# Kernel tuning notes

Measured on AMD Instinct MI355X. Metric: run time of the kernel, lower is better.

Reference implementation:

```python
import jax, jax.numpy as jnp
import numpy as np

N_HEADS = 16
K_CH = 1024 // N_HEADS  # 64
SCALE = 1.0 / np.sqrt(K_CH)


def setup_inputs() -> dict:
    key = jax.random.key(0)
    ks = jax.random.split(key, 10)
    B, C, T = 4, 1024, 2048
    Cout = 1024
    xavier = lambda k, o, i: jax.random.uniform(k, (o, i), jnp.float32, -1.0, 1.0) * np.sqrt(6.0 / (o + i))
    return {
        "x": jax.random.normal(ks[0], (B, C, T), jnp.float32),
        "c": jax.random.normal(ks[1], (B, C, T), jnp.float32),
        "Wq": xavier(ks[2], C, C), "bq": jnp.zeros((C,), jnp.float32),
        "Wk": xavier(ks[3], C, C), "bk": jnp.zeros((C,), jnp.float32),
        "Wv": xavier(ks[4], C, C), "bv": jnp.zeros((C,), jnp.float32),
        "Wo": xavier(ks[5], Cout, C), "bo": jnp.zeros((Cout,), jnp.float32),
    }


def reference(x, c, Wq, bq, Wk, bk, Wv, bv, Wo, bo):
    B, C, T = x.shape
    H, K = N_HEADS, K_CH
    # 1x1 Conv1d == per-timestep linear: [O,C] @ [B,C,T] -> [B,O,T]
    q = jnp.einsum('oc,bct->bot', Wq, x) + bq[None, :, None]
    k = jnp.einsum('oc,bct->bot', Wk, c) + bk[None, :, None]
    v = jnp.einsum('oc,bct->bot', Wv, c) + bv[None, :, None]
    # split heads: b (h k) t -> b h k t
    q = q.reshape(B, H, K, T)
    k = k.reshape(B, H, K, -1)
    v = v.reshape(B, H, K, -1)
    scores = jnp.einsum('bhkt,bhks->bhts', q, k) * SCALE  # [B,H,Tt,Ts]
    p = jax.nn.softmax(scores, axis=-1)
    out = jnp.einsum('bhts,bhks->bhkt', p, v)  # b h k t
    out = out.reshape(B, H * K, T)
    return jnp.einsum('oc,bct->bot', Wo, out) + bo[None, :, None]
```

## Files before the change

### kernel.cpp

```cpp
#include <hip/hip_runtime.h>
#include <stdint.h>

typedef __bf16 bf16x8 __attribute__((ext_vector_type(8)));
typedef float f32x4 __attribute__((ext_vector_type(4)));
typedef float f32x16 __attribute__((ext_vector_type(16)));
typedef unsigned u32x2 __attribute__((ext_vector_type(2)));
typedef unsigned u32x4 __attribute__((ext_vector_type(4)));

#define LOG2E 1.44269504088896340736f
#define ATT_SCALE 0.125f
#define CL (ATT_SCALE * LOG2E)
#define SWZ(row, colb) ((colb) ^ (((row) & 7) << 4))

#define GLOAD_LDS16(gp, lp)                                                  \
  __builtin_amdgcn_global_load_lds(                                          \
      (const __attribute__((address_space(1))) void*)(gp),                   \
      (__attribute__((address_space(3))) void*)(lp), 16, 0, 0)

__device__ __forceinline__ unsigned short f2bf(float f) {
  unsigned int x = __float_as_uint(f);
  x += 0x7fffu + ((x >> 16) & 1u);
  return (unsigned short)(x >> 16);
}

__device__ __forceinline__ float fexp2(float x) {
#if __has_builtin(__builtin_amdgcn_exp2f)
  return __builtin_amdgcn_exp2f(x);
#else
  return exp2f(x);
#endif
}

__device__ __forceinline__ unsigned cvtpk(float lo, float hi) {
  unsigned r;
  asm("v_cvt_pk_bf16_f32 %0, %1, %2" : "=v"(r) : "v"(lo), "v"(hi));
  return r;
}

__device__ __forceinline__ u32x2 plswap(unsigned a, unsigned b) {
  asm("v_permlane32_swap_b32 %0, %1" : "+v"(a), "+v"(b));
  u32x2 r;
  r[0] = a;
  r[1] = b;
  return r;
}

__global__ __launch_bounds__(256) void prep_inputs(
    const float* __restrict__ x, const float* __restrict__ c,
    const float* __restrict__ Wq, const float* __restrict__ Wk,
    const float* __restrict__ Wv, const float* __restrict__ Wo,
    unsigned short* __restrict__ xT, unsigned short* __restrict__ cT,
    unsigned short* __restrict__ wqb, unsigned short* __restrict__ wkb,
    unsigned short* __restrict__ wvb, unsigned short* __restrict__ wob) {
  const int C = 1024, T = 2048;
  int z = blockIdx.z;
  if (z >= 8) {
    int bi = blockIdx.y * 64 + blockIdx.x;
    long i = ((long)bi * 256 + threadIdx.x) * 8;
    int sel = (int)(i >> 20);
    const float* in = sel == 0 ? Wq : sel == 1 ? Wk : sel == 2 ? Wv : Wo;
    unsigned short* out = sel == 0 ? wqb : sel == 1 ? wkb : sel == 2 ? wvb : wob;
    float scale = sel == 0 ? CL : 1.0f;
    int off = (int)(i & 0xFFFFF);
    #pragma unroll
    for (int p = 0; p < 2; ++p) {
      float4 v = *(const float4*)(in + off + p * 4);
      ushort4 o;
      o.x = f2bf(v.x * scale); o.y = f2bf(v.y * scale);
      o.z = f2bf(v.z * scale); o.w = f2bf(v.w * scale);
      *(ushort4*)(out + off + p * 4) = o;
    }
    return;
  }
  __shared__ unsigned short tile[32][33];
  const float* in = (z < 4) ? x : c;
  unsigned short* out = (z < 4) ? xT : cT;
  int b = z & 3;
  int t0 = blockIdx.x * 32, c0 = blockIdx.y * 32;
  int tx = threadIdx.x & 31, ty = threadIdx.x >> 5;
  const float* src = in + ((size_t)b * C + c0) * T + t0;
  #pragma unroll
  for (int i = 0; i < 4; ++i) {
    int cc = ty + i * 8;
    tile[cc][tx] = f2bf(src[(size_t)cc * T + tx]);
  }
  __syncthreads();
  unsigned short* dst = out + ((size_t)b * T + t0) * C + c0;
  #pragma unroll
  for (int i = 0; i < 4; ++i) {
    int tt = ty + i * 8;
    dst[(size_t)tt * C + tx] = tile[tx][tt];
  }
}

template <int NT, int OUT_F32>
__device__ __forceinline__ void gemm_core128(
    const unsigned short* __restrict__ A, const unsigned short* __restrict__ B,
    void* __restrict__ Cv, const float* __restrict__ bias, int bias_is_m,
    float bs, int m0, int n0, int ldC) {
  __shared__ __align__(16) char lds[3 * 16384];
  const int tid = threadIdx.x;
  const int l = tid & 63, w = tid >> 6;
  const int g = l >> 4, j = l & 15;
  const int wr = w >> 1, wc = w & 1;

  const int r0 = tid >> 3;
  const int slotp = (tid & 7) ^ (r0 & 7);
  const int mloc = r0 * 2 + (slotp >> 2);
  const int kg = slotp & 3;
  const unsigned short* ga0 = A + (size_t)(m0 + mloc) * 1024 + kg * 8;
  const unsigned short* ga1 = A + (size_t)(m0 + 64 + mloc) * 1024 + kg * 8;
  const unsigned short* gb0 = B + (size_t)(n0 + mloc) * 1024 + kg * 8;
  const unsigned short* gb1 = B + (size_t)(n0 + 64 + mloc) * 1024 + kg * 8;

  auto stage = [&](char* buf) {
    GLOAD_LDS16(ga0, buf + tid * 16);
    GLOAD_LDS16(ga1, buf + 4096 + tid * 16);
    GLOAD_LDS16(gb0, buf + 8192 + tid * 16);
    GLOAD_LDS16(gb1, buf + 12288 + tid * 16);
    ga0 += 32; ga1 += 32; gb0 += 32; gb1 += 32;
  };

  f32x4 acc[4][4] = {};

  stage(lds);
  stage(lds + 16384);

  char* bufc = lds;
  char* bufs = lds + 2 * 16384;

  for (int t = 0; t < NT; ++t) {
    if (t == NT - 1) asm volatile("s_waitcnt vmcnt(0)" ::: "memory");
    else             asm volatile("s_waitcnt vmcnt(4)" ::: "memory");
    __builtin_amdgcn_s_barrier();
    asm volatile("" ::: "memory");
    if (t < NT - 2) stage(bufs);

    bf16x8 af[4], bfr[4];
    #pragma unroll
    for (int mf = 0; mf < 4; ++mf) {
      int m = wr * 64 + mf * 16 + j;
      int rp = m >> 1;
      int cb = ((m & 1) * 64 + g * 16) ^ ((rp & 7) << 4);
      af[mf] = *(const bf16x8*)(bufc + rp * 128 + cb);
    }
    #pragma unroll
    for (int nf = 0; nf < 4; ++nf) {
      int n = wc * 64 + nf * 16 + j;
      int rp = n >> 1;
      int cb = ((n & 1) * 64 + g * 16) ^ ((rp & 7) << 4);
      bfr[nf] = *(const bf16x8*)(bufc + 8192 + rp * 128 + cb);
    }
    #pragma unroll
    for (int mf = 0; mf < 4; ++mf)
      #pragma unroll
      for (int nf = 0; nf < 4; ++nf)
        acc[mf][nf] = __builtin_amdgcn_mfma_f32_16x16x32_bf16(af[mf], bfr[nf], acc[mf][nf], 0, 0, 0);

    bufc += 16384; if (bufc == lds + 49152) bufc = lds;
    bufs += 16384; if (bufs == lds + 49152) bufs = lds;
  }

  #pragma unroll
  for (int mf = 0; mf < 4; ++mf) {
    #pragma unroll
    for (int rr = 0; rr < 4; ++rr) {
      int m = m0 + wr * 64 + mf * 16 + g * 4 + rr;
      float bm = bias_is_m ? bias[m] * bs : 0.f;
      #pragma unroll
      for (int nf = 0; nf < 4; ++nf) {
        int n = n0 + wc * 64 + nf * 16 + j;
        float val = acc[mf][nf][rr] + bm + (bias_is_m ? 0.f : bias[n] * bs);
        if (OUT_F32) ((float*)Cv)[(size_t)m * ldC + n] = val;
        else ((unsigned short*)Cv)[(size_t)m * ldC + n] = f2bf(val);
      }
    }
  }
}

__global__ __launch_bounds__(256, 3) void qkv_gemm3(
    const unsigned short* __restrict__ xT, const unsigned short* __restrict__ cT,
    const unsigned short* __restrict__ wq, const unsigned short* __restrict__ wk,
    const unsigned short* __restrict__ wv,
    const float* __restrict__ bq, const float* __restrict__ bk,
    const float* __restrict__ bv,
    unsigned short* __restrict__ QT, unsigned short* __restrict__ KT,
    unsigned short* __restrict__ Vb) {
  const size_t sBT = (size_t)2048 * 1024;
  const int id = (blockIdx.x & 7) * 192 + (blockIdx.x >> 3);
  const int op = id >> 9;
  const int r = id & 511;
  const int z = r >> 7;
  const unsigned short *A, *B;
  unsigned short* Cp;
  const float* bias;
  int m0, n0, ldC, bias_is_m;
  float bs;
  if (op == 2) {
    n0 = (r & 15) * 128; m0 = ((r >> 4) & 7) * 128;
    A = wv; B = cT + z * sBT; Cp = Vb + z * (size_t)1024 * 2048;
    bias = bv; ldC = 2048; bias_is_m = 1; bs = 1.0f;
  } else {
    n0 = (r & 7) * 128; m0 = ((r >> 3) & 15) * 128;
    A = (op == 0 ? xT : cT) + z * sBT;
    B = (op == 0 ? wq : wk);
    Cp = (op == 0 ? QT : KT) + z * sBT;
    bias = (op == 0 ? bq : bk); ldC = 1024; bias_is_m = 0;
    bs = (op == 0) ? CL : 1.0f;
  }
  gemm_core128<32, 0>(A, B, Cp, bias, bias_is_m, bs, m0, n0, ldC);
}

__global__ __launch_bounds__(256, 3) void gemm_out3(
    const unsigned short* __restrict__ Wo, const unsigned short* __restrict__ OT,
    float* __restrict__ Out, const float* __restrict__ bias) {
  const size_t sBT = (size_t)2048 * 1024;
  const int id = (blockIdx.x & 7) * 64 + (blockIdx.x >> 3);
  const int z = id >> 7;
  const int m0 = ((id >> 4) & 7) * 128, n0 = (id & 15) * 128;
  gemm_core128<32, 1>(Wo, OT + z * sBT, Out + z * (size_t)1024 * 2048,
                      bias, 1, 1.0f, m0, n0, 2048);
}

__global__ __launch_bounds__(256, 4) void attn_kernel5(const unsigned short* __restrict__ QT,
                                                       const unsigned short* __restrict__ KT,
                                                       const unsigned short* __restrict__ V,
                                                       unsigned short* __restrict__ OT) {
  __shared__ __align__(16) char kv[2][16384];

  const int fid = blockIdx.x;
  const int xcd = fid & 7, idx = fid >> 3;
  const int bh = ((idx & 7) << 3) | xcd;
  const int tblk = idx >> 3;
  const int b = bh >> 4, h = bh & 15;

  const int tid = threadIdx.x;
  const int w = tid >> 6, l = tid & 63, lo5 = l & 31, hi = l >> 5;
  const int tq0 = tblk * 128 + w * 32;

  bf16x8 q[4];
  {
    const unsigned short* Qb = QT + ((size_t)(b * 2048 + tq0 + lo5)) * 1024 + h * 64 + hi * 8;
    #pragma unroll
    for (int kb = 0; kb < 4; ++kb) q[kb] = *(const bf16x8*)(Qb + kb * 16);
  }

  f32x16 o[2] = {};
  f32x16 ol = {};

  const unsigned one2 = 0x3F803F80u;
  const bf16x8 ones = __builtin_bit_cast(bf16x8, (u32x4){one2, one2, one2, one2});

  const int srow0 = tid >> 3, sslot = tid & 7;
  const unsigned short* Kg0 = KT + ((size_t)b * 2048) * 1024 + h * 64;
  const unsigned short* Vg0 = V + ((size_t)(b * 1024 + h * 64)) * 2048;

  auto stage = [&](int bsel, int s0) {
    char* Ks = kv[bsel];
    char* Vs = kv[bsel] + 8192;
    #pragma unroll
    for (int p = 0; p < 2; ++p) {
      int row = p * 32 + srow0;
      int ch = sslot ^ (row & 7);
      GLOAD_LDS16(Kg0 + (size_t)(s0 + row) * 1024 + ch * 8, Ks + (p * 256 + tid) * 16);
      GLOAD_LDS16(Vg0 + (size_t)row * 2048 + s0 + ch * 8, Vs + (p * 256 + tid) * 16);
    }
  };

  stage(0, 0);
  __syncthreads();

  for (int t = 0; t < 32; ++t) {
    int cur = t & 1;
    if (t < 31) stage(cur ^ 1, (t + 1) * 64);
    char* Ks = kv[cur];
    char* Vs = kv[cur] + 8192;

    f32x16 p0 = {}, p1 = {};
    __builtin_amdgcn_s_setprio(1);
    #pragma unroll
    for (int kb = 0; kb < 4; ++kb) {
      int r0 = lo5, r1 = 32 + lo5;
      bf16x8 ka0 = *(const bf16x8*)(Ks + r0 * 128 + SWZ(r0, kb * 32 + hi * 16));
      bf16x8 ka1 = *(const bf16x8*)(Ks + r1 * 128 + SWZ(r1, kb * 32 + hi * 16));
      p0 = __builtin_amdgcn_mfma_f32_32x32x16_bf16(ka0, q[kb], p0, 0, 0, 0);
      p1 = __builtin_amdgcn_mfma_f32_32x32x16_bf16(ka1, q[kb], p1, 0, 0, 0);
    }
    __builtin_amdgcn_s_setprio(0);

    #pragma unroll
    for (int r = 0; r < 16; ++r) p0[r] = fexp2(p0[r]);
    #pragma unroll
    for (int r = 0; r < 16; ++r) p1[r] = fexp2(p1[r]);

    u32x4 pa[4];
    {
      u32x2 ra = plswap(cvtpk(p0[0], p0[1]), cvtpk(p0[4], p0[5]));
      u32x2 rb = plswap(cvtpk(p0[2], p0[3]), cvtpk(p0[6], p0[7]));
      pa[0] = (u32x4){ra[0], rb[0], ra[1], rb[1]};
      u32x2 rc = plswap(cvtpk(p0[8], p0[9]), cvtpk(p0[12], p0[13]));
      u32x2 rd = plswap(cvtpk(p0[10], p0[11]), cvtpk(p0[14], p0[15]));
      pa[1] = (u32x4){rc[0], rd[0], rc[1], rd[1]};
      u32x2 re = plswap(cvtpk(p1[0], p1[1]), cvtpk(p1[4], p1[5]));
      u32x2 rf = plswap(cvtpk(p1[2], p1[3]), cvtpk(p1[6], p1[7]));
      pa[2] = (u32x4){re[0], rf[0], re[1], rf[1]};
      u32x2 rg = plswap(cvtpk(p1[8], p1[9]), cvtpk(p1[12], p1[13]));
      u32x2 rh = plswap(cvtpk(p1[10], p1[11]), cvtpk(p1[14], p1[15]));
      pa[3] = (u32x4){rg[0], rh[0], rg[1], rh[1]};
    }

    __builtin_amdgcn_s_setprio(1);
    #pragma unroll
    for (int sb = 0; sb < 4; ++sb) {
      bf16x8 pab = __builtin_bit_cast(bf16x8, pa[sb]);
      #pragma unroll
      for (int kb2 = 0; kb2 < 2; ++kb2) {
        int row = kb2 * 32 + lo5;
        bf16x8 vb = *(const bf16x8*)(Vs + row * 128 + SWZ(row, sb * 32 + hi * 16));
        o[kb2] = __builtin_amdgcn_mfma_f32_32x32x16_bf16(pab, vb, o[kb2], 0, 0, 0);
      }
      ol = __builtin_amdgcn_mfma_f32_32x32x16_bf16(pab, ones, ol, 0, 0, 0);
    }
    __builtin_amdgcn_s_setprio(0);
    __syncthreads();
  }

  unsigned short* Ob = OT + ((size_t)(b * 2048 + tq0)) * 1024 + h * 64 + lo5;
  #pragma unroll
  for (int r = 0; r < 16; ++r) {
    int srow = (r & 3) + 8 * (r >> 2) + 4 * hi;
    float inv = 1.0f / ol[r];
    Ob[(size_t)srow * 1024 + 0]  = f2bf(o[0][r] * inv);
    Ob[(size_t)srow * 1024 + 32] = f2bf(o[1][r] * inv);
  }
}

extern "C" void kernel_launch(void* const* d_in, const int* in_sizes, int n_in,
                              void* d_out, int out_size, void* d_ws, size_t ws_size,
                              hipStream_t stream) {
  const float* x  = (const float*)d_in[0];
  const float* c  = (const float*)d_in[1];
  const float* Wq = (const float*)d_in[2];
  const float* bq = (const float*)d_in[3];
  const float* Wk = (const float*)d_in[4];
  const float* bk = (const float*)d_in[5];
  const float* Wv = (const float*)d_in[6];
  const float* bv = (const float*)d_in[7];
  const float* Wo = (const float*)d_in[8];
  const float* bo = (const float*)d_in[9];

  const size_t MB = 1024 * 1024;
  char* ws = (char*)d_ws;
  unsigned short* wqb = (unsigned short*)(ws + 0 * MB);
  unsigned short* wkb = (unsigned short*)(ws + 2 * MB);
  unsigned short* wvb = (unsigned short*)(ws + 4 * MB);
  unsigned short* wob = (unsigned short*)(ws + 6 * MB);
  unsigned short* xT  = (unsigned short*)(ws + 8 * MB);
  unsigned short* cT  = (unsigned short*)(ws + 24 * MB);
  unsigned short* QT  = (unsigned short*)(ws + 40 * MB);
  unsigned short* KT  = (unsigned short*)(ws + 56 * MB);
  unsigned short* Vb  = (unsigned short*)(ws + 72 * MB);
  unsigned short* OT  = xT;

  prep_inputs<<<dim3(64, 32, 12), 256, 0, stream>>>(x, c, Wq, Wk, Wv, Wo,
                                                    xT, cT, wqb, wkb, wvb, wob);

  qkv_gemm3<<<dim3(1536), 256, 0, stream>>>(xT, cT, wqb, wkb, wvb, bq, bk, bv, QT, KT, Vb);

  attn_kernel5<<<dim3(1024), 256, 0, stream>>>(QT, KT, Vb, OT);

  gemm_out3<<<dim3(512), 256, 0, stream>>>(wob, OT, (float*)d_out, bo);
}
```

Baseline: 197.9 us.

## Triple-buffer K/V tiles in attention with one barrier and vmcnt-based waits

The attention kernel moves from double to triple buffering of the K/V LDS tiles. It prefetches two tiles ahead and syncs once per iteration using a partial s_waitcnt vmcnt plus a raw s_barrier, in place of __syncthreads at the end of each step. Staging addresses are now precomputed pointers advanced by increments, and the s_setprio hints are removed. The extra 16KB of LDS lowers the occupancy target from 4 to 3 blocks per CU in exchange for deeper load latency hiding.

```diff
diff --git a/kernel.cpp b/kernel.cpp
--- a/kernel.cpp
+++ b/kernel.cpp
@@ -222,11 +222,11 @@
                       bias, 1, 1.0f, m0, n0, 2048);
 }
 
-__global__ __launch_bounds__(256, 4) void attn_kernel5(const unsigned short* __restrict__ QT,
+__global__ __launch_bounds__(256, 3) void attn_kernel6(const unsigned short* __restrict__ QT,
                                                        const unsigned short* __restrict__ KT,
                                                        const unsigned short* __restrict__ V,
                                                        unsigned short* __restrict__ OT) {
-  __shared__ __align__(16) char kv[2][16384];
+  __shared__ __align__(16) char kv[3][16384];
 
   const int fid = blockIdx.x;
   const int xcd = fid & 7, idx = fid >> 3;
@@ -252,32 +252,39 @@
   const bf16x8 ones = __builtin_bit_cast(bf16x8, (u32x4){one2, one2, one2, one2});
 
   const int srow0 = tid >> 3, sslot = tid & 7;
-  const unsigned short* Kg0 = KT + ((size_t)b * 2048) * 1024 + h * 64;
-  const unsigned short* Vg0 = V + ((size_t)(b * 1024 + h * 64)) * 2048;
-
-  auto stage = [&](int bsel, int s0) {
-    char* Ks = kv[bsel];
-    char* Vs = kv[bsel] + 8192;
-    #pragma unroll
-    for (int p = 0; p < 2; ++p) {
-      int row = p * 32 + srow0;
-      int ch = sslot ^ (row & 7);
-      GLOAD_LDS16(Kg0 + (size_t)(s0 + row) * 1024 + ch * 8, Ks + (p * 256 + tid) * 16);
-      GLOAD_LDS16(Vg0 + (size_t)row * 2048 + s0 + ch * 8, Vs + (p * 256 + tid) * 16);
-    }
+  const int ch0 = sslot ^ (srow0 & 7);
+  const int ch1 = sslot ^ ((32 + srow0) & 7);
+  const unsigned short* kp0 = KT + ((size_t)(b * 2048 + srow0)) * 1024 + h * 64 + ch0 * 8;
+  const unsigned short* kp1 = KT + ((size_t)(b * 2048 + 32 + srow0)) * 1024 + h * 64 + ch1 * 8;
+  const unsigned short* vp0 = V + ((size_t)(b * 1024 + h * 64 + srow0)) * 2048 + ch0 * 8;
+  const unsigned short* vp1 = V + ((size_t)(b * 1024 + h * 64 + 32 + srow0)) * 2048 + ch1 * 8;
+
+  auto stage = [&](char* buf) {
+    GLOAD_LDS16(kp0, buf + tid * 16);
+    GLOAD_LDS16(kp1, buf + 4096 + tid * 16);
+    GLOAD_LDS16(vp0, buf + 8192 + tid * 16);
+    GLOAD_LDS16(vp1, buf + 12288 + tid * 16);
+    kp0 += 64 * 1024; kp1 += 64 * 1024;
+    vp0 += 64; vp1 += 64;
   };
 
-  stage(0, 0);
-  __syncthreads();
+  stage(kv[0]);
+  stage(kv[1]);
+
+  char* bufc = kv[0];
+  char* bufs = kv[2];
 
   for (int t = 0; t < 32; ++t) {
-    int cur = t & 1;
-    if (t < 31) stage(cur ^ 1, (t + 1) * 64);
-    char* Ks = kv[cur];
-    char* Vs = kv[cur] + 8192;
+    if (t == 31) asm volatile("s_waitcnt vmcnt(0)" ::: "memory");
+    else         asm volatile("s_waitcnt vmcnt(4)" ::: "memory");
+    __builtin_amdgcn_s_barrier();
+    asm volatile("" ::: "memory");
+    if (t < 30) stage(bufs);
+
+    const char* Ks = bufc;
+    const char* Vs = bufc + 8192;
 
     f32x16 p0 = {}, p1 = {};
-    __builtin_amdgcn_s_setprio(1);
     #pragma unroll
     for (int kb = 0; kb < 4; ++kb) {
       int r0 = lo5, r1 = 32 + lo5;
@@ -286,7 +293,6 @@
       p0 = __builtin_amdgcn_mfma_f32_32x32x16_bf16(ka0, q[kb], p0, 0, 0, 0);
       p1 = __builtin_amdgcn_mfma_f32_32x32x16_bf16(ka1, q[kb], p1, 0, 0, 0);
     }
-    __builtin_amdgcn_s_setprio(0);
 
     #pragma unroll
     for (int r = 0; r < 16; ++r) p0[r] = fexp2(p0[r]);
@@ -309,7 +315,6 @@
       pa[3] = (u32x4){rg[0], rh[0], rg[1], rh[1]};
     }
 
-    __builtin_amdgcn_s_setprio(1);
     #pragma unroll
     for (int sb = 0; sb < 4; ++sb) {
       bf16x8 pab = __builtin_bit_cast(bf16x8, pa[sb]);
@@ -321,8 +326,9 @@
       }
       ol = __builtin_amdgcn_mfma_f32_32x32x16_bf16(pab, ones, ol, 0, 0, 0);
     }
-    __builtin_amdgcn_s_setprio(0);
-    __syncthreads();
+
+    bufc += 16384; if (bufc == kv[0] + 49152) bufc = kv[0];
+    bufs += 16384; if (bufs == kv[0] + 49152) bufs = kv[0];
   }
 
   unsigned short* Ob = OT + ((size_t)(b * 2048 + tq0)) * 1024 + h * 64 + lo5;
@@ -367,7 +373,7 @@
 
   qkv_gemm3<<<dim3(1536), 256, 0, stream>>>(xT, cT, wqb, wkb, wvb, bq, bk, bv, QT, KT, Vb);
 
-  attn_kernel5<<<dim3(1024), 256, 0, stream>>>(QT, KT, Vb, OT);
+  attn_kernel6<<<dim3(1024), 256, 0, stream>>>(QT, KT, Vb, OT);
 
   gemm_out3<<<dim3(512), 256, 0, stream>>>(wob, OT, (float*)d_out, bo);
 }
```

Measured after the change: 192.3 us. 1.03x faster.
